# Performance work log

Measured on AMD Instinct MI355X. Metric: run time of the kernel, lower is better.

## Reference

```python
import jax, jax.numpy as jnp
import numpy as np

N = 1_000_000   # pose-graph nodes
E = 2_000_000   # edges (odometry + loop closures)
M = N - 1
L1, L2, L3, L4 = 1.0, 0.1, 1.0, 0.1  # loss weights
EPS = 1e-8

# ---- quaternion / Lie-group helpers (pypose convention: [x,y,z,w]) ----

def qmul(q, r):
    qv, qw = q[..., :3], q[..., 3:]
    rv, rw = r[..., :3], r[..., 3:]
    w = qw * rw - jnp.sum(qv * rv, axis=-1, keepdims=True)
    v = qw * rv + rw * qv + jnp.cross(qv, rv)
    return jnp.concatenate([v, w], axis=-1)

def qconj(q):  # inverse of a unit quaternion
    return jnp.concatenate([-q[..., :3], q[..., 3:]], axis=-1)

def qrot(q, v):  # rotate vector v by unit quaternion q
    qv, qw = q[..., :3], q[..., 3:]
    t = 2.0 * jnp.cross(qv, v)
    return v + qw * t + jnp.cross(qv, t)

def so3_log(q):  # SO3 -> so3 rotation vector phi
    v, w = q[..., :3], q[..., 3]
    n = jnp.linalg.norm(v, axis=-1)
    theta = 2.0 * jnp.arctan2(n, w)
    big = n > EPS
    k = jnp.where(big, theta / jnp.where(big, n, 1.0), 2.0 / jnp.where(jnp.abs(w) > EPS, w, 1.0))
    return v * k[..., None]

def se3_log(t, q):  # SE3 -> se3 = [tau(3), phi(3)] (translation first, pypose order)
    phi = so3_log(q)
    theta2 = jnp.sum(phi * phi, axis=-1)
    theta = jnp.sqrt(theta2)
    small = theta < 1e-4
    ts = jnp.where(small, 1.0, theta)
    # V^{-1} coefficient: 1/theta^2 - (1+cos)/(2 theta sin); Taylor -> 1/12
    coef = jnp.where(small, 1.0 / 12.0,
                     1.0 / jnp.where(small, 1.0, theta2)
                     - (1.0 + jnp.cos(ts)) / (2.0 * ts * jnp.sin(ts)))
    pxt = jnp.cross(phi, t)
    tau = t - 0.5 * pxt + coef[..., None] * jnp.cross(phi, pxt)  # V^{-1} t without 3x3 mats
    return jnp.concatenate([tau, phi], axis=-1)

def _unit_quat(key, n):
    q = jax.random.normal(key, (n, 4), dtype=jnp.float32)
    return q / jnp.linalg.norm(q, axis=-1, keepdims=True)

def setup_inputs() -> dict:
    key = jax.random.key(0)
    k = jax.random.split(key, 9)
    nodes = jnp.concatenate([jax.random.normal(k[0], (N, 3), jnp.float32), _unit_quat(k[1], N)], axis=-1)
    vels = jax.random.normal(k[2], (N, 3), jnp.float32)
    edges = jax.random.randint(k[3], (E, 2), 0, N, dtype=jnp.int32)
    poses = jnp.concatenate([jax.random.normal(k[4], (E, 3), jnp.float32), _unit_quat(k[5], E)], axis=-1)
    imu_drots = _unit_quat(k[6], M)
    imu_dtrans = 0.1 * jax.random.normal(k[7], (M, 3), jnp.float32)
    imu_dvels = 0.1 * jax.random.normal(k[8], (M, 3), jnp.float32)
    dts = jnp.full((M, 1), 0.05, dtype=jnp.float32)
    return dict(edges=edges, nodes=nodes, vels=vels, poses=poses,
                imu_drots=imu_drots, imu_dtrans=imu_dtrans, imu_dvels=imu_dvels, dts=dts)

def reference(edges, nodes, vels, poses, imu_drots, imu_dtrans, imu_dvels, dts):
    t_n, q_n = nodes[:, :3], nodes[:, 3:]
    # --- pose-graph residual: (poses^-1 o node1^-1 o node2).Log() ---
    n1 = nodes[edges[:, 0]]
    n2 = nodes[edges[:, 1]]
    t1, q1 = n1[:, :3], n1[:, 3:]
    t2, q2 = n2[:, :3], n2[:, 3:]
    tp, qp = poses[:, :3], poses[:, 3:]
    qi1 = qconj(q1)
    ti1 = -qrot(qi1, t1)           # node1^-1
    qa = qmul(qi1, q2)
    ta = ti1 + qrot(qi1, t2)       # node1^-1 o node2
    qip = qconj(qp)
    tip = -qrot(qip, tp)           # poses^-1
    qe = qmul(qip, qa)
    te = tip + qrot(qip, ta)
    pgerr = se3_log(te, qe)                                   # [E, 6]
    # --- adjacent velocity residual ---
    adjvelerr = imu_dvels - (vels[1:] - vels[:-1])            # [M, 3]
    # --- IMU rotation residual: (drot^-1 o R1^-1 o R2).Log() ---
    qre = qmul(qconj(imu_drots), qmul(qconj(q_n[:-1]), q_n[1:]))
    imuroterr = so3_log(qre)                                  # [M, 3]
    # --- translation/velocity residual ---
    transvelerr = (t_n[1:] - t_n[:-1]) - (vels[:-1] * dts + imu_dtrans)  # [M, 3]
    return jnp.concatenate([L1 * pgerr.ravel(), L2 * adjvelerr.ravel(),
                            L3 * imuroterr.ravel(), L4 * transvelerr.ravel()], axis=0)
```

## Files before the change

kernel.cpp:

```cpp
#include <hip/hip_runtime.h>
#include <math.h>

#define EPS_Q 1e-8f

struct F3 { float x, y, z; };
struct Q4 { F3 v; float w; };

__device__ __forceinline__ F3 add3(F3 a, F3 b){ return {a.x+b.x, a.y+b.y, a.z+b.z}; }
__device__ __forceinline__ F3 sub3(F3 a, F3 b){ return {a.x-b.x, a.y-b.y, a.z-b.z}; }
__device__ __forceinline__ F3 scal3(float s, F3 a){ return {s*a.x, s*a.y, s*a.z}; }
__device__ __forceinline__ float dot3(F3 a, F3 b){ return a.x*b.x + a.y*b.y + a.z*b.z; }
__device__ __forceinline__ F3 cross3(F3 a, F3 b){
    return { a.y*b.z - a.z*b.y, a.z*b.x - a.x*b.z, a.x*b.y - a.y*b.x };
}

__device__ __forceinline__ Q4 qmul(Q4 q, Q4 r){
    Q4 o;
    o.w = q.w*r.w - dot3(q.v, r.v);
    o.v = add3(add3(scal3(q.w, r.v), scal3(r.w, q.v)), cross3(q.v, r.v));
    return o;
}
__device__ __forceinline__ Q4 qconj(Q4 q){ return { {-q.v.x, -q.v.y, -q.v.z}, q.w }; }
__device__ __forceinline__ F3 qrot(Q4 q, F3 v){
    F3 t = scal3(2.0f, cross3(q.v, v));
    return add3(add3(v, scal3(q.w, t)), cross3(q.v, t));
}
__device__ __forceinline__ F3 so3_log(Q4 q){
    float n = sqrtf(dot3(q.v, q.v));
    float theta = 2.0f * atan2f(n, q.w);
    float k;
    if (n > EPS_Q) k = theta / n;
    else           k = 2.0f / ((fabsf(q.w) > EPS_Q) ? q.w : 1.0f);
    return scal3(k, q.v);
}

__global__ void edge_kernel(const int*   __restrict__ edges,
                            const float* __restrict__ nodes,
                            const float* __restrict__ poses,
                            float*       __restrict__ out,
                            int E)
{
    int e = blockIdx.x * blockDim.x + threadIdx.x;
    if (e >= E) return;

    int i = edges[2*(size_t)e];
    int j = edges[2*(size_t)e + 1];
    const float* n1 = nodes + 7*(size_t)i;
    const float* n2 = nodes + 7*(size_t)j;
    const float* p  = poses + 7*(size_t)e;

    F3 t1 = {n1[0], n1[1], n1[2]};  Q4 q1 = {{n1[3], n1[4], n1[5]}, n1[6]};
    F3 t2 = {n2[0], n2[1], n2[2]};  Q4 q2 = {{n2[3], n2[4], n2[5]}, n2[6]};
    F3 tp = {p[0],  p[1],  p[2]};   Q4 qp = {{p[3],  p[4],  p[5]},  p[6]};

    Q4 qi1 = qconj(q1);
    F3 ti1 = scal3(-1.0f, qrot(qi1, t1));
    Q4 qa  = qmul(qi1, q2);
    F3 ta  = add3(ti1, qrot(qi1, t2));

    Q4 qip = qconj(qp);
    F3 tip = scal3(-1.0f, qrot(qip, tp));
    Q4 qe  = qmul(qip, qa);
    F3 te  = add3(tip, qrot(qip, ta));

    F3 phi = so3_log(qe);
    float theta2 = dot3(phi, phi);
    float theta  = sqrtf(theta2);
    float coef;
    if (theta < 1e-4f) {
        coef = 1.0f / 12.0f;
    } else {
        coef = 1.0f / theta2 - (1.0f + cosf(theta)) / (2.0f * theta * sinf(theta));
    }
    F3 pxt = cross3(phi, te);
    F3 tau = add3(sub3(te, scal3(0.5f, pxt)), scal3(coef, cross3(phi, pxt)));

    float* o = out + 6*(size_t)e;
    o[0] = tau.x; o[1] = tau.y; o[2] = tau.z;
    o[3] = phi.x; o[4] = phi.y; o[5] = phi.z;
}

__global__ void node_kernel(const float* __restrict__ nodes,
                            const float* __restrict__ vels,
                            const float* __restrict__ imu_drots,
                            const float* __restrict__ imu_dtrans,
                            const float* __restrict__ imu_dvels,
                            const float* __restrict__ dts,
                            float*       __restrict__ out,
                            int M,
                            size_t off_adjvel, size_t off_imurot, size_t off_transvel)
{
    int m = blockIdx.x * blockDim.x + threadIdx.x;
    if (m >= M) return;

    const float* n0 = nodes + 7*(size_t)m;
    const float* n1 = nodes + 7*(size_t)(m+1);
    F3 t0 = {n0[0], n0[1], n0[2]};  Q4 q0 = {{n0[3], n0[4], n0[5]}, n0[6]};
    F3 t1 = {n1[0], n1[1], n1[2]};  Q4 q1 = {{n1[3], n1[4], n1[5]}, n1[6]};

    F3 v0 = {vels[3*(size_t)m],     vels[3*(size_t)m + 1], vels[3*(size_t)m + 2]};
    F3 v1 = {vels[3*(size_t)m + 3], vels[3*(size_t)m + 4], vels[3*(size_t)m + 5]};

    F3 dvm = {imu_dvels[3*(size_t)m], imu_dvels[3*(size_t)m + 1], imu_dvels[3*(size_t)m + 2]};
    F3 adjv = sub3(dvm, sub3(v1, v0));
    out[off_adjvel + 3*(size_t)m    ] = 0.1f * adjv.x;
    out[off_adjvel + 3*(size_t)m + 1] = 0.1f * adjv.y;
    out[off_adjvel + 3*(size_t)m + 2] = 0.1f * adjv.z;

    Q4 dr = {{imu_drots[4*(size_t)m], imu_drots[4*(size_t)m + 1], imu_drots[4*(size_t)m + 2]},
              imu_drots[4*(size_t)m + 3]};
    Q4 qre = qmul(qconj(dr), qmul(qconj(q0), q1));
    F3 rot = so3_log(qre);
    out[off_imurot + 3*(size_t)m    ] = rot.x;
    out[off_imurot + 3*(size_t)m + 1] = rot.y;
    out[off_imurot + 3*(size_t)m + 2] = rot.z;

    float dt = dts[m];
    F3 dtr = {imu_dtrans[3*(size_t)m], imu_dtrans[3*(size_t)m + 1], imu_dtrans[3*(size_t)m + 2]};
    F3 tv = sub3(sub3(t1, t0), add3(scal3(dt, v0), dtr));
    out[off_transvel + 3*(size_t)m    ] = 0.1f * tv.x;
    out[off_transvel + 3*(size_t)m + 1] = 0.1f * tv.y;
    out[off_transvel + 3*(size_t)m + 2] = 0.1f * tv.z;
}

extern "C" void kernel_launch(void* const* d_in, const int* in_sizes, int n_in,
                              void* d_out, int out_size, void* d_ws, size_t ws_size,
                              hipStream_t stream) {
    const int*   edges      = (const int*)  d_in[0];
    const float* nodes      = (const float*)d_in[1];
    const float* vels       = (const float*)d_in[2];
    const float* poses      = (const float*)d_in[3];
    const float* imu_drots  = (const float*)d_in[4];
    const float* imu_dtrans = (const float*)d_in[5];
    const float* imu_dvels  = (const float*)d_in[6];
    const float* dts        = (const float*)d_in[7];
    float* out = (float*)d_out;

    const int E = in_sizes[0] / 2;
    const int M = in_sizes[7];

    const size_t off_adjvel   = 6*(size_t)E;
    const size_t off_imurot   = off_adjvel + 3*(size_t)M;
    const size_t off_transvel = off_imurot + 3*(size_t)M;

    const int BLK = 256;
    edge_kernel<<<(E + BLK - 1) / BLK, BLK, 0, stream>>>(edges, nodes, poses, out, E);
    node_kernel<<<(M + BLK - 1) / BLK, BLK, 0, stream>>>(nodes, vels, imu_drots, imu_dtrans,
                                                         imu_dvels, dts, out, M,
                                                         off_adjvel, off_imurot, off_transvel);
}
```

Baseline: 270.2 us.

## Pad nodes to float4 pairs and fuse edge/node kernels with nontemporal memory ops

Adds a pre-pass that copies the 7-float node records into a padded 8-float (two float4) workspace, so the random gathers in the edge path become two aligned vector loads instead of seven scalar loads. The edge and node residual kernels are merged into one launch, and each edge thread now handles two edges to put more gathers in flight. Streaming loads and stores are marked nontemporal to keep them from polluting cache. The cost is an extra pass over the node array plus the workspace writes, and the new path only runs when the workspace is large enough.

```diff
diff --git a/kernel.cpp b/kernel.cpp
--- a/kernel.cpp
+++ b/kernel.cpp
@@ -13,7 +13,6 @@
 __device__ __forceinline__ F3 cross3(F3 a, F3 b){
     return { a.y*b.z - a.z*b.y, a.z*b.x - a.x*b.z, a.x*b.y - a.y*b.x };
 }
-
 __device__ __forceinline__ Q4 qmul(Q4 q, Q4 r){
     Q4 o;
     o.w = q.w*r.w - dot3(q.v, r.v);
@@ -34,25 +33,9 @@
     return scal3(k, q.v);
 }
 
-__global__ void edge_kernel(const int*   __restrict__ edges,
-                            const float* __restrict__ nodes,
-                            const float* __restrict__ poses,
-                            float*       __restrict__ out,
-                            int E)
-{
-    int e = blockIdx.x * blockDim.x + threadIdx.x;
-    if (e >= E) return;
-
-    int i = edges[2*(size_t)e];
-    int j = edges[2*(size_t)e + 1];
-    const float* n1 = nodes + 7*(size_t)i;
-    const float* n2 = nodes + 7*(size_t)j;
-    const float* p  = poses + 7*(size_t)e;
-
-    F3 t1 = {n1[0], n1[1], n1[2]};  Q4 q1 = {{n1[3], n1[4], n1[5]}, n1[6]};
-    F3 t2 = {n2[0], n2[1], n2[2]};  Q4 q2 = {{n2[3], n2[4], n2[5]}, n2[6]};
-    F3 tp = {p[0],  p[1],  p[2]};   Q4 qp = {{p[3],  p[4],  p[5]},  p[6]};
-
+__device__ __forceinline__ void edge_compute(F3 t1, Q4 q1, F3 t2, Q4 q2,
+                                             F3 tp, Q4 qp, float* __restrict__ o)
+{
     Q4 qi1 = qconj(q1);
     F3 ti1 = scal3(-1.0f, qrot(qi1, t1));
     Q4 qa  = qmul(qi1, q2);
@@ -75,9 +58,134 @@
     F3 pxt = cross3(phi, te);
     F3 tau = add3(sub3(te, scal3(0.5f, pxt)), scal3(coef, cross3(phi, pxt)));
 
-    float* o = out + 6*(size_t)e;
-    o[0] = tau.x; o[1] = tau.y; o[2] = tau.z;
-    o[3] = phi.x; o[4] = phi.y; o[5] = phi.z;
+    __builtin_nontemporal_store(tau.x, o + 0);
+    __builtin_nontemporal_store(tau.y, o + 1);
+    __builtin_nontemporal_store(tau.z, o + 2);
+    __builtin_nontemporal_store(phi.x, o + 3);
+    __builtin_nontemporal_store(phi.y, o + 4);
+    __builtin_nontemporal_store(phi.z, o + 5);
+}
+
+__global__ void pad_nodes_kernel(const float* __restrict__ nodes,
+                                 float4* __restrict__ pn, int N)
+{
+    int i = blockIdx.x * blockDim.x + threadIdx.x;
+    if (i >= N) return;
+    const float* s = nodes + 7*(size_t)i;
+    float4 a = { s[0], s[1], s[2], s[3] };
+    float4 b = { s[4], s[5], s[6], 0.0f };
+    pn[2*(size_t)i    ] = a;
+    pn[2*(size_t)i + 1] = b;
+}
+
+__global__ void fused_main(const int*    __restrict__ edges,
+                           const float4* __restrict__ pn,
+                           const float*  __restrict__ poses,
+                           const float*  __restrict__ vels,
+                           const float*  __restrict__ imu_drots,
+                           const float*  __restrict__ imu_dtrans,
+                           const float*  __restrict__ imu_dvels,
+                           const float*  __restrict__ dts,
+                           float*        __restrict__ out,
+                           int E, int M, int edge_threads)
+{
+    int tid = blockIdx.x * blockDim.x + threadIdx.x;
+    if (tid < edge_threads) {
+        int e0 = 2*tid;
+        int e1 = e0 + 1;
+        bool has1 = (e1 < E);
+        int e1s = has1 ? e1 : e0;
+
+        int i0 = __builtin_nontemporal_load(edges + 2*(size_t)e0);
+        int j0 = __builtin_nontemporal_load(edges + 2*(size_t)e0 + 1);
+        int i1 = __builtin_nontemporal_load(edges + 2*(size_t)e1s);
+        int j1 = __builtin_nontemporal_load(edges + 2*(size_t)e1s + 1);
+
+        float4 na0 = pn[2*(size_t)i0], na1 = pn[2*(size_t)i0 + 1];
+        float4 nb0 = pn[2*(size_t)j0], nb1 = pn[2*(size_t)j0 + 1];
+        float4 nc0 = pn[2*(size_t)i1], nc1 = pn[2*(size_t)i1 + 1];
+        float4 nd0 = pn[2*(size_t)j1], nd1 = pn[2*(size_t)j1 + 1];
+
+        const float* p0 = poses + 7*(size_t)e0;
+        const float* p1 = poses + 7*(size_t)e1s;
+        float pp0[7], pp1[7];
+        #pragma unroll
+        for (int k = 0; k < 7; ++k) pp0[k] = __builtin_nontemporal_load(p0 + k);
+        #pragma unroll
+        for (int k = 0; k < 7; ++k) pp1[k] = __builtin_nontemporal_load(p1 + k);
+
+        {
+            F3 t1 = {na0.x, na0.y, na0.z};  Q4 q1 = {{na0.w, na1.x, na1.y}, na1.z};
+            F3 t2 = {nb0.x, nb0.y, nb0.z};  Q4 q2 = {{nb0.w, nb1.x, nb1.y}, nb1.z};
+            F3 tp = {pp0[0], pp0[1], pp0[2]}; Q4 qp = {{pp0[3], pp0[4], pp0[5]}, pp0[6]};
+            edge_compute(t1, q1, t2, q2, tp, qp, out + 6*(size_t)e0);
+        }
+        if (has1) {
+            F3 t1 = {nc0.x, nc0.y, nc0.z};  Q4 q1 = {{nc0.w, nc1.x, nc1.y}, nc1.z};
+            F3 t2 = {nd0.x, nd0.y, nd0.z};  Q4 q2 = {{nd0.w, nd1.x, nd1.y}, nd1.z};
+            F3 tp = {pp1[0], pp1[1], pp1[2]}; Q4 qp = {{pp1[3], pp1[4], pp1[5]}, pp1[6]};
+            edge_compute(t1, q1, t2, q2, tp, qp, out + 6*(size_t)e1);
+        }
+    } else {
+        int m = tid - edge_threads;
+        if (m >= M) return;
+
+        const size_t off_adjvel   = 6*(size_t)E;
+        const size_t off_imurot   = off_adjvel + 3*(size_t)M;
+        const size_t off_transvel = off_imurot + 3*(size_t)M;
+
+        float4 n0a = pn[2*(size_t)m    ], n0b = pn[2*(size_t)m + 1];
+        float4 n1a = pn[2*(size_t)m + 2], n1b = pn[2*(size_t)m + 3];
+        F3 t0 = {n0a.x, n0a.y, n0a.z};  Q4 q0 = {{n0a.w, n0b.x, n0b.y}, n0b.z};
+        F3 t1 = {n1a.x, n1a.y, n1a.z};  Q4 q1 = {{n1a.w, n1b.x, n1b.y}, n1b.z};
+
+        F3 v0 = {vels[3*(size_t)m],     vels[3*(size_t)m + 1], vels[3*(size_t)m + 2]};
+        F3 v1 = {vels[3*(size_t)m + 3], vels[3*(size_t)m + 4], vels[3*(size_t)m + 5]};
+
+        F3 dvm = { __builtin_nontemporal_load(imu_dvels + 3*(size_t)m),
+                   __builtin_nontemporal_load(imu_dvels + 3*(size_t)m + 1),
+                   __builtin_nontemporal_load(imu_dvels + 3*(size_t)m + 2) };
+        F3 adjv = sub3(dvm, sub3(v1, v0));
+        __builtin_nontemporal_store(0.1f * adjv.x, out + off_adjvel + 3*(size_t)m);
+        __builtin_nontemporal_store(0.1f * adjv.y, out + off_adjvel + 3*(size_t)m + 1);
+        __builtin_nontemporal_store(0.1f * adjv.z, out + off_adjvel + 3*(size_t)m + 2);
+
+        const float4 drv = ((const float4*)imu_drots)[m];
+        Q4 dr = {{drv.x, drv.y, drv.z}, drv.w};
+        Q4 qre = qmul(qconj(dr), qmul(qconj(q0), q1));
+        F3 rot = so3_log(qre);
+        __builtin_nontemporal_store(rot.x, out + off_imurot + 3*(size_t)m);
+        __builtin_nontemporal_store(rot.y, out + off_imurot + 3*(size_t)m + 1);
+        __builtin_nontemporal_store(rot.z, out + off_imurot + 3*(size_t)m + 2);
+
+        float dt = dts[m];
+        F3 dtr = { __builtin_nontemporal_load(imu_dtrans + 3*(size_t)m),
+                   __builtin_nontemporal_load(imu_dtrans + 3*(size_t)m + 1),
+                   __builtin_nontemporal_load(imu_dtrans + 3*(size_t)m + 2) };
+        F3 tv = sub3(sub3(t1, t0), add3(scal3(dt, v0), dtr));
+        __builtin_nontemporal_store(0.1f * tv.x, out + off_transvel + 3*(size_t)m);
+        __builtin_nontemporal_store(0.1f * tv.y, out + off_transvel + 3*(size_t)m + 1);
+        __builtin_nontemporal_store(0.1f * tv.z, out + off_transvel + 3*(size_t)m + 2);
+    }
+}
+
+__global__ void edge_kernel(const int*   __restrict__ edges,
+                            const float* __restrict__ nodes,
+                            const float* __restrict__ poses,
+                            float*       __restrict__ out,
+                            int E)
+{
+    int e = blockIdx.x * blockDim.x + threadIdx.x;
+    if (e >= E) return;
+    int i = edges[2*(size_t)e];
+    int j = edges[2*(size_t)e + 1];
+    const float* n1 = nodes + 7*(size_t)i;
+    const float* n2 = nodes + 7*(size_t)j;
+    const float* p  = poses + 7*(size_t)e;
+    F3 t1 = {n1[0], n1[1], n1[2]};  Q4 q1 = {{n1[3], n1[4], n1[5]}, n1[6]};
+    F3 t2 = {n2[0], n2[1], n2[2]};  Q4 q2 = {{n2[3], n2[4], n2[5]}, n2[6]};
+    F3 tp = {p[0],  p[1],  p[2]};   Q4 qp = {{p[3],  p[4],  p[5]},  p[6]};
+    edge_compute(t1, q1, t2, q2, tp, qp, out + 6*(size_t)e);
 }
 
 __global__ void node_kernel(const float* __restrict__ nodes,
@@ -92,21 +200,17 @@
 {
     int m = blockIdx.x * blockDim.x + threadIdx.x;
     if (m >= M) return;
-
     const float* n0 = nodes + 7*(size_t)m;
     const float* n1 = nodes + 7*(size_t)(m+1);
     F3 t0 = {n0[0], n0[1], n0[2]};  Q4 q0 = {{n0[3], n0[4], n0[5]}, n0[6]};
     F3 t1 = {n1[0], n1[1], n1[2]};  Q4 q1 = {{n1[3], n1[4], n1[5]}, n1[6]};
-
     F3 v0 = {vels[3*(size_t)m],     vels[3*(size_t)m + 1], vels[3*(size_t)m + 2]};
     F3 v1 = {vels[3*(size_t)m + 3], vels[3*(size_t)m + 4], vels[3*(size_t)m + 5]};
-
     F3 dvm = {imu_dvels[3*(size_t)m], imu_dvels[3*(size_t)m + 1], imu_dvels[3*(size_t)m + 2]};
     F3 adjv = sub3(dvm, sub3(v1, v0));
     out[off_adjvel + 3*(size_t)m    ] = 0.1f * adjv.x;
     out[off_adjvel + 3*(size_t)m + 1] = 0.1f * adjv.y;
     out[off_adjvel + 3*(size_t)m + 2] = 0.1f * adjv.z;
-
     Q4 dr = {{imu_drots[4*(size_t)m], imu_drots[4*(size_t)m + 1], imu_drots[4*(size_t)m + 2]},
               imu_drots[4*(size_t)m + 3]};
     Q4 qre = qmul(qconj(dr), qmul(qconj(q0), q1));
@@ -114,7 +218,6 @@
     out[off_imurot + 3*(size_t)m    ] = rot.x;
     out[off_imurot + 3*(size_t)m + 1] = rot.y;
     out[off_imurot + 3*(size_t)m + 2] = rot.z;
-
     float dt = dts[m];
     F3 dtr = {imu_dtrans[3*(size_t)m], imu_dtrans[3*(size_t)m + 1], imu_dtrans[3*(size_t)m + 2]};
     F3 tv = sub3(sub3(t1, t0), add3(scal3(dt, v0), dtr));
@@ -137,15 +240,27 @@
     float* out = (float*)d_out;
 
     const int E = in_sizes[0] / 2;
+    const int N = in_sizes[1] / 7;
     const int M = in_sizes[7];
 
-    const size_t off_adjvel   = 6*(size_t)E;
-    const size_t off_imurot   = off_adjvel + 3*(size_t)M;
-    const size_t off_transvel = off_imurot + 3*(size_t)M;
-
     const int BLK = 256;
-    edge_kernel<<<(E + BLK - 1) / BLK, BLK, 0, stream>>>(edges, nodes, poses, out, E);
-    node_kernel<<<(M + BLK - 1) / BLK, BLK, 0, stream>>>(nodes, vels, imu_drots, imu_dtrans,
-                                                         imu_dvels, dts, out, M,
-                                                         off_adjvel, off_imurot, off_transvel);
-}
+    const size_t need = 2 * (size_t)N * sizeof(float4);
+
+    if (ws_size >= need) {
+        float4* pn = (float4*)d_ws;
+        pad_nodes_kernel<<<(N + BLK - 1) / BLK, BLK, 0, stream>>>(nodes, pn, N);
+        const int edge_threads = (E + 1) / 2;
+        const long long total = (long long)edge_threads + M;
+        fused_main<<<(int)((total + BLK - 1) / BLK), BLK, 0, stream>>>(
+            edges, pn, poses, vels, imu_drots, imu_dtrans, imu_dvels, dts,
+            out, E, M, edge_threads);
+    } else {
+        const size_t off_adjvel   = 6*(size_t)E;
+        const size_t off_imurot   = off_adjvel + 3*(size_t)M;
+        const size_t off_transvel = off_imurot + 3*(size_t)M;
+        edge_kernel<<<(E + BLK - 1) / BLK, BLK, 0, stream>>>(edges, nodes, poses, out, E);
+        node_kernel<<<(M + BLK - 1) / BLK, BLK, 0, stream>>>(nodes, vels, imu_drots, imu_dtrans,
+                                                             imu_dvels, dts, out, M,
+                                                             off_adjvel, off_imurot, off_transvel);
+    }
+}
```

New measurement: 301.1 us. 1.11x slower.
